# Kernel tuning notes

Hardware: AMD Instinct MI355X
Metric: run time of the kernel (lower is better)

Reference implementation:

```python
import jax, jax.numpy as jnp
import numpy as np

N_SLOTS = 524288
DIM_MEM = 128
DIM_IN = 1024
SHIFT_RADIUS = 3
EPS = 1e-8  # torch cosine_similarity eps


def setup_inputs() -> dict:
    key = jax.random.key(0)
    k1, k2, k3, k4, k5 = jax.random.split(key, 5)
    n_factors = DIM_MEM + 1 + 1 + (2 * SHIFT_RADIUS + 1) + 1  # 138
    return {
        "input_from_controller": jax.random.normal(k1, (DIM_IN,), dtype=jnp.float32),
        "previous_weighting": jax.random.uniform(k2, (N_SLOTS,), dtype=jnp.float32),
        "memory": jax.random.normal(k3, (N_SLOTS, DIM_MEM), dtype=jnp.float32),
        "W_wf": jax.random.normal(k4, (DIM_IN, n_factors), dtype=jnp.float32) * 0.02,
        "b_wf": jax.random.normal(k5, (n_factors,), dtype=jnp.float32) * 0.02,
    }


def _get_weighting(input_from_controller, previous_weighting, memory, W_wf, b_wf):
    factors = input_from_controller @ W_wf + b_wf  # [138]
    M = DIM_MEM
    key_v = factors[:M]                       # [M]
    key_s = factors[M]                        # scalar (beta)
    gate = jax.nn.softmax(factors[M + 1:M + 2])      # size-1 softmax -> 1.0 (faithful)
    shift_w = jax.nn.softmax(factors[M + 2:M + 2 + 2 * SHIFT_RADIUS + 1])  # [2r+1]
    sharpening = jax.nn.relu(factors[-1]) + 1.0

    # content addressing: cosine similarity of each memory row with key_v
    mem_norm = jnp.maximum(jnp.linalg.norm(memory, axis=1), EPS)  # [N]
    key_norm = jnp.maximum(jnp.linalg.norm(key_v), EPS)
    content_w = (memory @ key_v) / (mem_norm * key_norm)          # [N]
    content_w = jax.nn.softmax(key_s * content_w)

    gated_w = content_w * gate[0] + (1.0 - gate[0]) * previous_weighting

    # circular convolution: shifted[i] = sum_j gated[(i - r + j) % N] * shift_w[j]
    shifted_w = jnp.zeros_like(gated_w)
    for j in range(2 * SHIFT_RADIUS + 1):  # small fixed tap count (7)
        shifted_w = shifted_w + shift_w[j] * jnp.roll(gated_w, SHIFT_RADIUS - j)

    pw = shifted_w ** sharpening
    return pw / pw.sum()


def reference(input_from_controller, previous_weighting, memory, W_wf, b_wf):
    w = _get_weighting(input_from_controller, previous_weighting, memory, W_wf, b_wf)
    read_vector = w @ memory  # read head forward
    return read_vector
```

## Files before the change

### kernel.cpp

```cpp
#include <hip/hip_runtime.h>
#include <math.h>

#define N_SLOTS 524288
#define DIM_MEM 128
#define DIM_IN 1024
#define NFACT 138
#define EPSF 1e-8f
#define CPB 4
#define ROWS_PC 64
#define NPAIR 70
#define PADH 33
#define NBLK (N_SLOTS / (CPB * ROWS_PC))
#define PSTRIDE 132


__global__ __launch_bounds__(256) void k_factors(const float* __restrict__ x,
                                                 const float* __restrict__ W,
                                                 const float* __restrict__ b,
                                                 float* __restrict__ factors) {
    int j = threadIdx.x;
    int i0 = blockIdx.x * 32;
    if (j < NFACT) {
        float acc = 0.f;
        #pragma unroll 8
        for (int i = i0; i < i0 + 32; ++i)
            acc = fmaf(x[i], W[(size_t)i * NFACT + j], acc);
        if (blockIdx.x == 0) acc += b[j];
        atomicAdd(&factors[j], acc);
    }
}

__global__ void k_derived(const float* __restrict__ f, float* __restrict__ d) {
    int l = threadIdx.x;
    float v = f[l] * f[l] + f[l + 64] * f[l + 64];
    for (int off = 32; off; off >>= 1) v += __shfl_xor(v, off, 64);
    if (l == 0) {
        float key_norm = fmaxf(sqrtf(v), EPSF);
        d[0] = f[128] / key_norm;
        float m = f[130];
        for (int j = 1; j < 7; ++j) m = fmaxf(m, f[130 + j]);
        float e[7], s = 0.f;
        for (int j = 0; j < 7; ++j) { e[j] = expf(f[130 + j] - m); s += e[j]; }
        for (int j = 0; j < 7; ++j) d[1 + j] = e[j] / s;
        d[8] = fmaxf(f[137], 0.f) + 1.f;
    }
}

__global__ __launch_bounds__(256) void k_main(const float* __restrict__ mem,
                                              const float* __restrict__ keyv,
                                              const float* __restrict__ der,
                                              float* __restrict__ partials) {
    __shared__ float2 part2[NPAIR * PADH];
    __shared__ float e_sh[NPAIR];
    __shared__ float w_sh[ROWS_PC];
    __shared__ float colpart[8][DIM_MEM];
    __shared__ float psum[8];

    const int tid  = threadIdx.x;
    const int lane = tid & 31;
    const int hw   = tid >> 5;
    const float4* mem4 = (const float4*)mem;
    const float4 k4 = ((const float4*)keyv)[lane];
    const float d0 = der[0];
    const float sharp = der[8];
    float sw[7];
    #pragma unroll
    for (int d = 0; d < 7; ++d) sw[d] = der[1 + d];

    float4 acc = make_float4(0.f, 0.f, 0.f, 0.f);
    float wsum = 0.f;

    float4 bufA[8], bufB[8], haloA, haloB;
    const int base = blockIdx.x * (CPB * ROWS_PC);

    {
        const int r0 = base, rbase = r0 + hw * 8;
        #pragma unroll
        for (int j = 0; j < 8; ++j)
            bufA[j] = mem4[(size_t)(rbase + j) * 32 + lane];
        if (hw < 6) {
            int hr = (hw < 3) ? (r0 - 3 + hw) : (r0 + ROWS_PC + (hw - 3));
            hr &= (N_SLOTS - 1);
            haloA = mem4[(size_t)hr * 32 + lane];
        }
    }

    #pragma unroll
    for (int c = 0; c < CPB; ++c) {
        float4* cur   = (c & 1) ? bufB : bufA;
        float4* nxt   = (c & 1) ? bufA : bufB;
        float4& curh  = (c & 1) ? haloB : haloA;
        float4& nxth  = (c & 1) ? haloA : haloB;

        if (c + 1 < CPB) {
            const int r0 = base + (c + 1) * ROWS_PC, rbase = r0 + hw * 8;
            #pragma unroll
            for (int j = 0; j < 8; ++j)
                nxt[j] = mem4[(size_t)(rbase + j) * 32 + lane];
            if (hw < 6) {
                int hr = (hw < 3) ? (r0 - 3 + hw) : (r0 + ROWS_PC + (hw - 3));
                hr &= (N_SLOTS - 1);
                nxth = mem4[(size_t)hr * 32 + lane];
            }
        }

        #pragma unroll
        for (int j = 0; j < 8; ++j) {
            float dp = cur[j].x * k4.x + cur[j].y * k4.y + cur[j].z * k4.z + cur[j].w * k4.w;
            float np = cur[j].x * cur[j].x + cur[j].y * cur[j].y + cur[j].z * cur[j].z + cur[j].w * cur[j].w;
            part2[(3 + hw * 8 + j) * PADH + lane] = make_float2(dp, np);
        }
        if (hw < 6) {
            int p = (hw < 3) ? hw : (64 + hw);
            float dp = curh.x * k4.x + curh.y * k4.y + curh.z * k4.z + curh.w * k4.w;
            float np = curh.x * curh.x + curh.y * curh.y + curh.z * curh.z + curh.w * curh.w;
            part2[p * PADH + lane] = make_float2(dp, np);
        }
        __syncthreads();

        if (tid < NPAIR) {
            const float2* q = &part2[tid * PADH];
            float d = 0.f, n = 0.f;
            #pragma unroll
            for (int l = 0; l < 32; ++l) { float2 v = q[l]; d += v.x; n += v.y; }
            e_sh[tid] = __expf(d0 * d / fmaxf(sqrtf(n), EPSF));
        }
        __syncthreads();

        if (tid < ROWS_PC) {
            float t = 0.f;
            #pragma unroll
            for (int d = 0; d < 7; ++d) t = fmaf(sw[d], e_sh[tid + d], t);
            w_sh[tid] = __expf(sharp * __logf(t));
        }
        __syncthreads();

        #pragma unroll
        for (int j = 0; j < 8; ++j) {
            float w = w_sh[hw * 8 + j];
            acc.x = fmaf(w, cur[j].x, acc.x);
            acc.y = fmaf(w, cur[j].y, acc.y);
            acc.z = fmaf(w, cur[j].z, acc.z);
            acc.w = fmaf(w, cur[j].w, acc.w);
            wsum += w;
        }
    }

    ((float4*)colpart[hw])[lane] = acc;
    if (lane == 0) psum[hw] = wsum;
    __syncthreads();
    float* slot = partials + (size_t)blockIdx.x * PSTRIDE;
    if (tid < DIM_MEM) {
        float s = 0.f;
        #pragma unroll
        for (int h = 0; h < 8; ++h) s += colpart[h][tid];
        slot[tid] = s;
    }
    if (tid == 0) {
        float s = 0.f;
        #pragma unroll
        for (int h = 0; h < 8; ++h) s += psum[h];
        slot[128] = s;
    }
}

__global__ void k_final(const float* __restrict__ partials,
                        float* __restrict__ out) {
    const int c = blockIdx.x, t = threadIdx.x;
    float s = 0.f, p = 0.f;
    for (int b = t; b < NBLK; b += 64) {
        s += partials[(size_t)b * PSTRIDE + c];
        p += partials[(size_t)b * PSTRIDE + 128];
    }
    for (int off = 32; off; off >>= 1) {
        s += __shfl_xor(s, off, 64);
        p += __shfl_xor(p, off, 64);
    }
    if (t == 0) out[c] = s / p;
}

extern "C" void kernel_launch(void* const* d_in, const int* in_sizes, int n_in,
                              void* d_out, int out_size, void* d_ws, size_t ws_size,
                              hipStream_t stream) {
    const float* x   = (const float*)d_in[0];
    const float* mem = (const float*)d_in[2];
    const float* W   = (const float*)d_in[3];
    const float* b   = (const float*)d_in[4];
    float* out = (float*)d_out;

    char* ws = (char*)d_ws;
    float* factors  = (float*)ws;
    float* derived  = (float*)(ws + 1024);
    float* partials = (float*)(ws + 4096);

    hipMemsetAsync(ws, 0, 4096, stream);

    k_factors<<<DIM_IN / 32, 256, 0, stream>>>(x, W, b, factors);
    k_derived<<<1, 64, 0, stream>>>(factors, derived);
    k_main<<<NBLK, 256, 0, stream>>>(mem, factors, derived, partials);
    k_final<<<DIM_MEM, 64, 0, stream>>>(partials, out);
}
```

Before: 385.7 us.

## Drop register double-buffering in k_main for higher occupancy and fewer barriers

The main kernel drops the explicit register double-buffer of memory rows and asks the compiler for 8 waves per SIMD through launch_bounds, so latency is hidden by more resident blocks rather than by in-thread prefetch. Each 32-lane row group is pre-reduced with a lane shuffle before writing to shared memory, which halves the shared partials. The float2 array is split into separate dot and norm arrays. The content-weight step and the shift-convolution step are merged so one barrier per chunk goes away. The risk is that less in-flight load per thread is not fully made up by the extra occupancy. The merged step also relies on threads 0-63 running as one wave64 when they read halo entries written by other lanes.

```diff
diff --git a/kernel.cpp b/kernel.cpp
--- a/kernel.cpp
+++ b/kernel.cpp
@@ -9,7 +9,7 @@
 #define CPB 4
 #define ROWS_PC 64
 #define NPAIR 70
-#define PADH 33
+#define PADS 17
 #define NBLK (N_SLOTS / (CPB * ROWS_PC))
 #define PSTRIDE 132
 
@@ -46,11 +46,12 @@
     }
 }
 
-__global__ __launch_bounds__(256) void k_main(const float* __restrict__ mem,
-                                              const float* __restrict__ keyv,
-                                              const float* __restrict__ der,
-                                              float* __restrict__ partials) {
-    __shared__ float2 part2[NPAIR * PADH];
+__global__ __launch_bounds__(256, 8) void k_main(const float* __restrict__ mem,
+                                                 const float* __restrict__ keyv,
+                                                 const float* __restrict__ der,
+                                                 float* __restrict__ partials) {
+    __shared__ float dotp[NPAIR * PADS];
+    __shared__ float n2p [NPAIR * PADS];
     __shared__ float e_sh[NPAIR];
     __shared__ float w_sh[ROWS_PC];
     __shared__ float colpart[8][DIM_MEM];
@@ -62,86 +63,81 @@
     const float4* mem4 = (const float4*)mem;
     const float4 k4 = ((const float4*)keyv)[lane];
     const float d0 = der[0];
-    const float sharp = der[8];
-    float sw[7];
-    #pragma unroll
-    for (int d = 0; d < 7; ++d) sw[d] = der[1 + d];
 
     float4 acc = make_float4(0.f, 0.f, 0.f, 0.f);
     float wsum = 0.f;
-
-    float4 bufA[8], bufB[8], haloA, haloB;
     const int base = blockIdx.x * (CPB * ROWS_PC);
 
-    {
-        const int r0 = base, rbase = r0 + hw * 8;
+    for (int c = 0; c < CPB; ++c) {
+        const int r0 = base + c * ROWS_PC;
+        const float4* src = mem4 + ((size_t)(r0 + hw * 8)) * 32 + lane;
+
+        float4 row[8];
         #pragma unroll
-        for (int j = 0; j < 8; ++j)
-            bufA[j] = mem4[(size_t)(rbase + j) * 32 + lane];
+        for (int j = 0; j < 8; ++j) row[j] = src[(size_t)j * 32];
+        float4 hrow;
         if (hw < 6) {
             int hr = (hw < 3) ? (r0 - 3 + hw) : (r0 + ROWS_PC + (hw - 3));
             hr &= (N_SLOTS - 1);
-            haloA = mem4[(size_t)hr * 32 + lane];
+            hrow = mem4[(size_t)hr * 32 + lane];
         }
-    }
-
-    #pragma unroll
-    for (int c = 0; c < CPB; ++c) {
-        float4* cur   = (c & 1) ? bufB : bufA;
-        float4* nxt   = (c & 1) ? bufA : bufB;
-        float4& curh  = (c & 1) ? haloB : haloA;
-        float4& nxth  = (c & 1) ? haloA : haloB;
-
-        if (c + 1 < CPB) {
-            const int r0 = base + (c + 1) * ROWS_PC, rbase = r0 + hw * 8;
-            #pragma unroll
-            for (int j = 0; j < 8; ++j)
-                nxt[j] = mem4[(size_t)(rbase + j) * 32 + lane];
-            if (hw < 6) {
-                int hr = (hw < 3) ? (r0 - 3 + hw) : (r0 + ROWS_PC + (hw - 3));
-                hr &= (N_SLOTS - 1);
-                nxth = mem4[(size_t)hr * 32 + lane];
+        #pragma unroll
+        for (int j = 0; j < 8; ++j) {
+            float dp = row[j].x * k4.x + row[j].y * k4.y + row[j].z * k4.z + row[j].w * k4.w;
+            float np = row[j].x * row[j].x + row[j].y * row[j].y + row[j].z * row[j].z + row[j].w * row[j].w;
+            dp += __shfl_xor(dp, 16, 32);
+            np += __shfl_xor(np, 16, 32);
+            if (lane < 16) {
+                int p = 3 + hw * 8 + j;
+                dotp[p * PADS + lane] = dp;
+                n2p [p * PADS + lane] = np;
             }
         }
-
-        #pragma unroll
-        for (int j = 0; j < 8; ++j) {
-            float dp = cur[j].x * k4.x + cur[j].y * k4.y + cur[j].z * k4.z + cur[j].w * k4.w;
-            float np = cur[j].x * cur[j].x + cur[j].y * cur[j].y + cur[j].z * cur[j].z + cur[j].w * cur[j].w;
-            part2[(3 + hw * 8 + j) * PADH + lane] = make_float2(dp, np);
-        }
         if (hw < 6) {
-            int p = (hw < 3) ? hw : (64 + hw);
-            float dp = curh.x * k4.x + curh.y * k4.y + curh.z * k4.z + curh.w * k4.w;
-            float np = curh.x * curh.x + curh.y * curh.y + curh.z * curh.z + curh.w * curh.w;
-            part2[p * PADH + lane] = make_float2(dp, np);
+            float dp = hrow.x * k4.x + hrow.y * k4.y + hrow.z * k4.z + hrow.w * k4.w;
+            float np = hrow.x * hrow.x + hrow.y * hrow.y + hrow.z * hrow.z + hrow.w * hrow.w;
+            dp += __shfl_xor(dp, 16, 32);
+            np += __shfl_xor(np, 16, 32);
+            if (lane < 16) {
+                int p = (hw < 3) ? hw : (64 + hw);
+                dotp[p * PADS + lane] = dp;
+                n2p [p * PADS + lane] = np;
+            }
         }
         __syncthreads();
 
-        if (tid < NPAIR) {
-            const float2* q = &part2[tid * PADH];
-            float d = 0.f, n = 0.f;
+        if (tid < 64) {
+            float dsum = 0.f, nsum = 0.f;
             #pragma unroll
-            for (int l = 0; l < 32; ++l) { float2 v = q[l]; d += v.x; n += v.y; }
-            e_sh[tid] = __expf(d0 * d / fmaxf(sqrtf(n), EPSF));
-        }
-        __syncthreads();
-
-        if (tid < ROWS_PC) {
+            for (int l = 0; l < 16; ++l) {
+                dsum += dotp[tid * PADS + l];
+                nsum += n2p [tid * PADS + l];
+            }
+            e_sh[tid] = __expf(d0 * dsum / fmaxf(sqrtf(nsum), EPSF));
+            if (tid < 6) {
+                int p = tid + 64;
+                float d2 = 0.f, n2 = 0.f;
+                #pragma unroll
+                for (int l = 0; l < 16; ++l) {
+                    d2 += dotp[p * PADS + l];
+                    n2 += n2p [p * PADS + l];
+                }
+                e_sh[p] = __expf(d0 * d2 / fmaxf(sqrtf(n2), EPSF));
+            }
             float t = 0.f;
             #pragma unroll
-            for (int d = 0; d < 7; ++d) t = fmaf(sw[d], e_sh[tid + d], t);
-            w_sh[tid] = __expf(sharp * __logf(t));
+            for (int d = 0; d < 7; ++d) t = fmaf(der[1 + d], e_sh[tid + d], t);
+            w_sh[tid] = __expf(der[8] * __logf(t));
         }
         __syncthreads();
 
         #pragma unroll
         for (int j = 0; j < 8; ++j) {
             float w = w_sh[hw * 8 + j];
-            acc.x = fmaf(w, cur[j].x, acc.x);
-            acc.y = fmaf(w, cur[j].y, acc.y);
-            acc.z = fmaf(w, cur[j].z, acc.z);
-            acc.w = fmaf(w, cur[j].w, acc.w);
+            acc.x = fmaf(w, row[j].x, acc.x);
+            acc.y = fmaf(w, row[j].y, acc.y);
+            acc.z = fmaf(w, row[j].z, acc.z);
+            acc.w = fmaf(w, row[j].w, acc.w);
             wsum += w;
         }
     }
```

Measured after the change: 395.1 us. +2.5%, slower.
